# Performance work log

Hardware: AMD Instinct MI355X
Metric: run time of the kernel (lower is better)

The kernel has to match this reference:

```python
import jax, jax.numpy as jnp
import numpy as np

B, CIN, COUT, SDIM, RES, K = 8, 512, 512, 512, 64, 3
AFF_SCALE = 1.0 / np.sqrt(SDIM)          # LinearAct: 1/sqrt(in_features)
CONV_SCALE = 1.0 / np.sqrt(CIN * K * K)  # ModulatedConv2d: 1/sqrt(in*k*k)
LRELU_GAIN = np.sqrt(2.0)                # bias_act 'lrelu' default gain


def setup_inputs() -> dict:
    key = jax.random.key(0)
    k = jax.random.split(key, 5)
    x = jax.random.normal(k[0], (B, CIN, RES, RES), dtype=jnp.float32)
    w = jax.random.normal(k[1], (B, SDIM), dtype=jnp.float32)
    noise = jax.random.normal(k[2], (B, 1, RES, RES), dtype=jnp.float32)
    affine_w = jax.random.normal(k[3], (CIN, SDIM), dtype=jnp.float32)
    affine_b = jnp.ones((CIN,), dtype=jnp.float32)          # bias.data.fill_(1.0)
    conv_w = jax.random.normal(k[4], (COUT, CIN, K, K), dtype=jnp.float32)
    noise_scale = jnp.asarray(0.1, dtype=jnp.float32)        # InjectNoise.scale (nonzero for a meaningful test)
    bias = jnp.zeros((COUT,), dtype=jnp.float32)
    return {"x": x, "w": w, "noise": noise, "affine_w": affine_w,
            "affine_b": affine_b, "conv_w": conv_w,
            "noise_scale": noise_scale, "bias": bias}


def reference(x, w, noise, affine_w, affine_b, conv_w, noise_scale, bias):
    # affine (LinearAct, act='linear'): style = w @ (W*scale)^T + b
    style = jnp.einsum('bs,cs->bc', w, affine_w * AFF_SCALE) + affine_b  # [B, CIN]

    # modulate + demodulate: per-sample weight [B, COUT, CIN, K, K]
    wt = conv_w[None] * style[:, None, :, None, None] * CONV_SCALE
    d = jax.lax.rsqrt(jnp.sum(wt * wt, axis=(2, 3, 4), keepdims=True) + 1e-8)
    wt = wt * d

    # grouped conv (groups=B) == per-sample conv; flip_weight=True -> plain correlation
    def conv_one(xi, wi):
        return jax.lax.conv_general_dilated(
            xi[None], wi, window_strides=(1, 1), padding=[(1, 1), (1, 1)],
            dimension_numbers=('NCHW', 'OIHW', 'NCHW'))[0]

    y = jax.vmap(conv_one)(x, wt)  # [B, COUT, RES, RES]

    # noise -> bias -> lrelu(0.2) * sqrt(2)
    y = y + noise * noise_scale
    y = jax.nn.leaky_relu(y + bias[None, :, None, None], 0.2) * LRELU_GAIN
    return y
```

## Files before the change

kernel.cpp:

```cpp
#include <hip/hip_runtime.h>
#include <hip/hip_bf16.h>

typedef unsigned short u16;

#define BATCH 8
#define CIN 512
#define COUT 512
#define SDIM 512
#define RES 64
#define PIX (RES * RES)
#define PPIX 4356
#define PANEL_E 139392

__device__ __constant__ static const float kAffScale  = 0.04419417382415922f;
__device__ __constant__ static const float kConvScale = 0.014731391274719742f;
__device__ __constant__ static const float kGain      = 1.4142135623730951f;

typedef __bf16 bf16x8 __attribute__((ext_vector_type(8)));
typedef float  f32x4  __attribute__((ext_vector_type(4)));

__global__ void style_k(const float* __restrict__ w, const float* __restrict__ aw,
                        const float* __restrict__ ab, float* __restrict__ style) {
  int tid = blockIdx.x * 256 + threadIdx.x;
  int b = tid >> 9, c = tid & 511;
  const float* wp = w + b * SDIM;
  const float* ap = aw + c * SDIM;
  float s = 0.0f;
  for (int k = 0; k < SDIM; ++k) s += wp[k] * ap[k];
  style[tid] = s * kAffScale + ab[c];
}

__global__ void cw2_k(const float* __restrict__ cw, float* __restrict__ cw2) {
  int tid = blockIdx.x * 256 + threadIdx.x;
  const float* p = cw + tid * 9;
  float s = 0.0f;
  #pragma unroll
  for (int t = 0; t < 9; ++t) { float v = p[t]; s += v * v; }
  cw2[tid] = s;
}

__global__ void fac_k(const float* __restrict__ style, const float* __restrict__ cw2,
                      float* __restrict__ fac) {
  int wid  = blockIdx.x * 4 + (threadIdx.x >> 6);
  int lane = threadIdx.x & 63;
  int b = wid >> 9, o = wid & 511;
  const float* st = style + b * CIN;
  const float* c2 = cw2 + o * CIN;
  float s = 0.0f;
  for (int i = lane; i < CIN; i += 64) { float sv = st[i]; s += sv * sv * c2[i]; }
  #pragma unroll
  for (int off = 32; off; off >>= 1) s += __shfl_xor(s, off);
  if (lane == 0) {
    float d = rsqrtf(s * kConvScale * kConvScale + 1e-8f);
    fac[wid] = d * kConvScale;
  }
}

__global__ void wcast_k(const float* __restrict__ cw, u16* __restrict__ wbt) {
  int tid = blockIdx.x * 256 + threadIdx.x;
  int o = tid >> 9, i = tid & 511;
  const float* p = cw + tid * 9;
  #pragma unroll
  for (int t = 0; t < 9; ++t) {
    __hip_bfloat16 h = __float2bfloat16(p[t]);
    wbt[((size_t)(t * 16 + (i >> 5)) * 512 + o) * 32 + (i & 31)] = *(u16*)&h;
  }
}

__global__ void bz_k(u16* __restrict__ xst) {
  int idx = blockIdx.x * 256 + threadIdx.x;
  if (idx >= 128 * PPIX) return;
  int pan = idx / PPIX, pix = idx - pan * PPIX;
  int h = pix / 66, w = pix - h * 66;
  if (h == 0 || h == 65 || w == 0 || w == 65) {
    u16* p = xst + (size_t)pan * PANEL_E + (size_t)pix * 32;
    int4 z = make_int4(0, 0, 0, 0);
    ((int4*)p)[0] = z; ((int4*)p)[1] = z; ((int4*)p)[2] = z; ((int4*)p)[3] = z;
  }
}

__global__ void modx_k(const float* __restrict__ x, const float* __restrict__ style,
                       u16* __restrict__ xst) {
  __shared__ float t[64][65];
  int b  = blockIdx.z;
  int it = blockIdx.y * 64;
  int pt = blockIdx.x * 64;
  int tp = threadIdx.x & 63;
  int tr = threadIdx.x >> 6;
  for (int r = tr; r < 64; r += 4) {
    int i = it + r;
    t[r][tp] = x[(b * CIN + i) * PIX + pt + tp] * style[b * CIN + i];
  }
  __syncthreads();
  int i = it + tp;
  size_t pbase = (size_t)(b * 16 + (i >> 5)) * PANEL_E + (i & 31);
  for (int r = tr; r < 64; r += 4) {
    int pix = pt + r, h = pix >> 6, w = pix & 63;
    __hip_bfloat16 hh = __float2bfloat16(t[tp][r]);
    xst[pbase + (size_t)((h + 1) * 66 + (w + 1)) * 32] = *(u16*)&hh;
  }
}

__launch_bounds__(512, 2)
__global__ void gemm_k(const u16* __restrict__ wbt, const u16* __restrict__ xst,
                       const float* __restrict__ fac, const float* __restrict__ noise,
                       const float* __restrict__ nscale_p, const float* __restrict__ bias,
                       float* __restrict__ y) {
  __shared__ __align__(16) u16 lds[75264];

  const int tid = threadIdx.x;
  const int bid = blockIdx.x;
  const int swz = (bid & 7) * 32 + (bid >> 3);
  const int mt = swz >> 7;
  const int nt = swz & 127;
  const int b  = nt >> 4;
  const int pimg  = (nt & 15) * 256;
  const int hbase = pimg >> 6;

  const int lane = tid & 63;
  const int wv = tid >> 6;
  const int wm = wv >> 2;
  const int wn = wv & 3;
  const int l15 = lane & 15, l4 = lane >> 4;
  const int pwn = (wn + 1) * 66 + l15;

  int aElem[8];
  #pragma unroll
  for (int mi = 0; mi < 8; ++mi) {
    int arow = wm * 128 + mi * 16 + l15;
    aElem[mi] = arow * 32 + ((l4 ^ ((arow >> 1) & 3)) << 3);
  }

  const int sgE = ((tid & 3) ^ ((tid >> 3) & 3)) << 3;
  int aoffE[2];
  #pragma unroll
  for (int p = 0; p < 2; ++p)
    aoffE[p] = (mt * 256 + ((p * 512 + tid) >> 2)) * 32 + sgE;

  auto stA = [&](int panel, int ring) {
    const u16* pan = wbt + ((size_t)panel << 14);
    #pragma unroll
    for (int p = 0; p < 2; ++p) {
      __builtin_amdgcn_global_load_lds(
          (const __attribute__((address_space(1))) void*)(pan + aoffE[p]),
          (__attribute__((address_space(3))) void*)(&lds[ring * 8192 + (p * 512 + tid) * 8]),
          16, 0, 0);
    }
  };

  auto stHalo = [&](int cbn) {
    const int dst0 = 24576 + (cbn & 1) * 25344;
    const size_t srcPan = (size_t)(b * 16 + cbn * 2) * PANEL_E + (size_t)(hbase * 66) * 32;
    #pragma unroll
    for (int pass = 0; pass < 6; ++pass) {
      int c = pass * 512 + tid;
      int kh = c >= 1584 ? 1 : 0;
      int r = c - (kh ? 1584 : 0);
      int p = r >> 2;
      int sg = (c & 3) ^ ((p >> 1) & 3);
      const u16* src = xst + srcPan + (size_t)kh * PANEL_E + p * 32 + sg * 8;
      __builtin_amdgcn_global_load_lds(
          (const __attribute__((address_space(1))) void*)src,
          (__attribute__((address_space(3))) void*)(&lds[dst0 + c * 8]), 16, 0, 0);
    }
    if (tid < 96) {
      int c = 3072 + tid;
      int p = (c - 1584) >> 2;
      int sg = (c & 3) ^ ((p >> 1) & 3);
      const u16* src = xst + srcPan + (size_t)PANEL_E + p * 32 + sg * 8;
      __builtin_amdgcn_global_load_lds(
          (const __attribute__((address_space(1))) void*)src,
          (__attribute__((address_space(3))) void*)(&lds[dst0 + c * 8]), 16, 0, 0);
    }
  };

  f32x4 acc[8][4];
  #pragma unroll
  for (int i = 0; i < 8; ++i)
    #pragma unroll
    for (int j = 0; j < 4; ++j) acc[i][j] = (f32x4){0.f, 0.f, 0.f, 0.f};

  stHalo(0);
  stA(0, 0);
  stA(1, 1);
  asm volatile("s_waitcnt vmcnt(2)" ::: "memory");
  __builtin_amdgcn_s_barrier();

#define PH(IDX) {                                                              \
    constexpr int tap_ = (IDX) >> 1, kh_ = (IDX) & 1;                          \
    constexpr int rr_ = (IDX) % 3;                                             \
    constexpr int nI_ = (IDX) + 2;                                             \
    constexpr int tapS_ = (nI_ % 18) >> 1, khS_ = (nI_ % 18) & 1;              \
    constexpr int rw_ = nI_ % 3;                                               \
    constexpr int dy_ = tap_ / 3 - 1, dx_ = tap_ % 3 - 1;                      \
    const int sb_ = 24576 + (cb & 1) * 25344 + kh_ * 12672;                    \
    bf16x8 bfr[4], af03[4], af47[4];                                           \
    _Pragma("unroll") for (int ni = 0; ni < 4; ++ni) {                         \
      int prow = pwn + (dy_ * 66 + dx_ + 1 + ni * 16);                         \
      int sl = (l4 ^ ((prow >> 1) & 3)) << 3;                                  \
      bfr[ni] = *(const bf16x8*)&lds[sb_ + prow * 32 + sl];                    \
    }                                                                          \
    _Pragma("unroll") for (int j = 0; j < 4; ++j)                              \
      af03[j] = *(const bf16x8*)&lds[rr_ * 8192 + aElem[j]];                   \
    __builtin_amdgcn_sched_barrier(0);    \
    _Pragma("unroll") for (int j = 0; j < 4; ++j)                              \
      af47[j] = *(const bf16x8*)&lds[rr_ * 8192 + aElem[4 + j]];               \
    stA(tapS_ * 16 + khS_ + ((nI_ >= 18) ? cbw : cb) * 2, rw_);                \
    if ((IDX) == 15) stHalo(cbw);                                              \
    __builtin_amdgcn_s_barrier();                                              \
    asm volatile("s_waitcnt lgkmcnt(4)" ::: "memory");                         \
    __builtin_amdgcn_sched_barrier(0);                                         \
    __builtin_amdgcn_s_setprio(1);                                             \
    _Pragma("unroll") for (int j = 0; j < 4; ++j)                              \
      _Pragma("unroll") for (int ni = 0; ni < 4; ++ni)                         \
        acc[j][ni] = __builtin_amdgcn_mfma_f32_16x16x32_bf16(af03[j], bfr[ni], acc[j][ni], 0, 0, 0); \
    __builtin_amdgcn_s_setprio(0);                                             \
    asm volatile("s_waitcnt lgkmcnt(0)" ::: "memory");                         \
    __builtin_amdgcn_sched_barrier(0);                                         \
    __builtin_amdgcn_s_setprio(1);                                             \
    _Pragma("unroll") for (int j = 0; j < 4; ++j)                              \
      _Pragma("unroll") for (int ni = 0; ni < 4; ++ni)                         \
        acc[4 + j][ni] = __builtin_amdgcn_mfma_f32_16x16x32_bf16(af47[j], bfr[ni], acc[4 + j][ni], 0, 0, 0); \
    __builtin_amdgcn_s_setprio(0);                                             \
    if ((IDX) == 15 || (IDX) == 16) {                                          \
      asm volatile("s_waitcnt vmcnt(8)" ::: "memory");                         \
    } else {                                                                   \
      asm volatile("s_waitcnt vmcnt(2)" ::: "memory");                         \
    }                                                                          \
    __builtin_amdgcn_s_barrier();                                              \
  }

  for (int cb = 0; cb < 8; ++cb) {
    const int cbw = (cb == 7) ? 0 : cb + 1;
    PH(0)  PH(1)  PH(2)  PH(3)  PH(4)  PH(5)  PH(6)  PH(7)  PH(8)
    PH(9)  PH(10) PH(11) PH(12) PH(13) PH(14) PH(15) PH(16) PH(17)
  }
#undef PH

  const float ns = nscale_p[0];
  float nz[4];
  #pragma unroll
  for (int ni = 0; ni < 4; ++ni) {
    int pix = pimg + wn * 64 + ni * 16 + l15;
    nz[ni] = noise[b * PIX + pix] * ns;
  }
  #pragma unroll
  for (int mi = 0; mi < 8; ++mi) {
    int o = mt * 256 + wm * 128 + mi * 16 + l4 * 4;
    f32x4 fv = *(const f32x4*)&fac[b * COUT + o];
    f32x4 bv = *(const f32x4*)&bias[o];
    #pragma unroll
    for (int r = 0; r < 4; ++r) {
      float* yp = y + (size_t)(b * COUT + o + r) * PIX + pimg + wn * 64 + l15;
      #pragma unroll
      for (int ni = 0; ni < 4; ++ni) {
        float v = acc[mi][ni][r] * fv[r] + nz[ni] + bv[r];
        v = (v > 0.0f ? v : 0.2f * v) * kGain;
        yp[ni * 16] = v;
      }
    }
  }
}

extern "C" void kernel_launch(void* const* d_in, const int* in_sizes, int n_in,
                              void* d_out, int out_size, void* d_ws, size_t ws_size,
                              hipStream_t stream) {
  const float* x      = (const float*)d_in[0];
  const float* w      = (const float*)d_in[1];
  const float* noise  = (const float*)d_in[2];
  const float* aff_w  = (const float*)d_in[3];
  const float* aff_b  = (const float*)d_in[4];
  const float* conv_w = (const float*)d_in[5];
  const float* nscale = (const float*)d_in[6];
  const float* bias   = (const float*)d_in[7];
  float* y = (float*)d_out;

  char* ws = (char*)d_ws;
  float* style = (float*)(ws);
  float* fac   = (float*)(ws + 16384);
  float* cw2   = (float*)(ws + 32768);
  u16*   wbt   = (u16*)(ws + 1081600);
  u16*   xst   = (u16*)(ws + 5800192);

  style_k<<<16, 256, 0, stream>>>(w, aff_w, aff_b, style);
  cw2_k<<<1024, 256, 0, stream>>>(conv_w, cw2);
  fac_k<<<1024, 256, 0, stream>>>(style, cw2, fac);
  wcast_k<<<1024, 256, 0, stream>>>(conv_w, wbt);
  bz_k<<<(128 * PPIX + 255) / 256, 256, 0, stream>>>(xst);
  modx_k<<<dim3(64, 8, 8), 256, 0, stream>>>(x, style, xst);
  gemm_k<<<256, 512, 0, stream>>>(wbt, xst, fac, noise, nscale, bias, y);
}
```

Baseline: 191.5 us.

## Load conv activations directly from global into registers instead of staging halo in LDS

Drops the LDS halo staging of the activation panel. Each wave now loads its B fragments straight from global memory into a three-deep register ring (q0/q1/q2), issued two half-phases ahead. The LDS A-weight ring is reorganised to hold both kh halves per tap. This saves LDS capacity and LDS read traffic, but it replaces the shared halo reuse with per-wave global/L2 loads that re-read the overlapping taps, and it keeps more registers live.

```diff
diff --git a/kernel.cpp b/kernel.cpp
--- a/kernel.cpp
+++ b/kernel.cpp
@@ -106,7 +106,7 @@
                        const float* __restrict__ fac, const float* __restrict__ noise,
                        const float* __restrict__ nscale_p, const float* __restrict__ bias,
                        float* __restrict__ y) {
-  __shared__ __align__(16) u16 lds[75264];
+  __shared__ __align__(16) u16 Ab[49152];
 
   const int tid = threadIdx.x;
   const int bid = blockIdx.x;
@@ -122,7 +122,6 @@
   const int wm = wv >> 2;
   const int wn = wv & 3;
   const int l15 = lane & 15, l4 = lane >> 4;
-  const int pwn = (wn + 1) * 66 + l15;
 
   int aElem[8];
   #pragma unroll
@@ -137,105 +136,94 @@
   for (int p = 0; p < 2; ++p)
     aoffE[p] = (mt * 256 + ((p * 512 + tid) >> 2)) * 32 + sgE;
 
-  auto stA = [&](int panel, int ring) {
+  const int pB0 = ((hbase + wn + 1) * 66 + l15 + 1) * 32 + l4 * 8;
+
+  auto stA = [&](int panel, int ring, int khS) {
     const u16* pan = wbt + ((size_t)panel << 14);
     #pragma unroll
     for (int p = 0; p < 2; ++p) {
       __builtin_amdgcn_global_load_lds(
           (const __attribute__((address_space(1))) void*)(pan + aoffE[p]),
-          (__attribute__((address_space(3))) void*)(&lds[ring * 8192 + (p * 512 + tid) * 8]),
+          (__attribute__((address_space(3))) void*)(&Ab[ring * 16384 + khS * 8192 + (p * 512 + tid) * 8]),
           16, 0, 0);
     }
   };
 
-  auto stHalo = [&](int cbn) {
-    const int dst0 = 24576 + (cbn & 1) * 25344;
-    const size_t srcPan = (size_t)(b * 16 + cbn * 2) * PANEL_E + (size_t)(hbase * 66) * 32;
-    #pragma unroll
-    for (int pass = 0; pass < 6; ++pass) {
-      int c = pass * 512 + tid;
-      int kh = c >= 1584 ? 1 : 0;
-      int r = c - (kh ? 1584 : 0);
-      int p = r >> 2;
-      int sg = (c & 3) ^ ((p >> 1) & 3);
-      const u16* src = xst + srcPan + (size_t)kh * PANEL_E + p * 32 + sg * 8;
-      __builtin_amdgcn_global_load_lds(
-          (const __attribute__((address_space(1))) void*)src,
-          (__attribute__((address_space(3))) void*)(&lds[dst0 + c * 8]), 16, 0, 0);
-    }
-    if (tid < 96) {
-      int c = 3072 + tid;
-      int p = (c - 1584) >> 2;
-      int sg = (c & 3) ^ ((p >> 1) & 3);
-      const u16* src = xst + srcPan + (size_t)PANEL_E + p * 32 + sg * 8;
-      __builtin_amdgcn_global_load_lds(
-          (const __attribute__((address_space(1))) void*)src,
-          (__attribute__((address_space(3))) void*)(&lds[dst0 + c * 8]), 16, 0, 0);
-    }
-  };
-
   f32x4 acc[8][4];
   #pragma unroll
   for (int i = 0; i < 8; ++i)
     #pragma unroll
     for (int j = 0; j < 4; ++j) acc[i][j] = (f32x4){0.f, 0.f, 0.f, 0.f};
 
-  stHalo(0);
-  stA(0, 0);
-  stA(1, 1);
-  asm volatile("s_waitcnt vmcnt(2)" ::: "memory");
+  bf16x8 q0[4], q1[4], q2[4];
+
+#define BISSUE(SN, TAPB, CBB, KHB) {                                           \
+    const u16* pb_ = xst + (size_t)(b * 16 + (CBB) * 2 + (KHB)) * PANEL_E      \
+        + ((((TAPB) / 3) - 1) * 66 + ((TAPB) % 3) - 1) * 32 + pB0;             \
+    _Pragma("unroll") for (int ni = 0; ni < 4; ++ni)                           \
+      SN[ni] = *(const bf16x8*)(pb_ + ni * 512);                               \
+  }
+
+#define MFMA16(AF, BQ, MOFF)                                                   \
+    _Pragma("unroll") for (int j = 0; j < 4; ++j)                              \
+      _Pragma("unroll") for (int ni = 0; ni < 4; ++ni)                         \
+        acc[(MOFF) + j][ni] = __builtin_amdgcn_mfma_f32_16x16x32_bf16(         \
+            AF[j], BQ[ni], acc[(MOFF) + j][ni], 0, 0, 0);
+
+  {
+    const int cbw0 = 0;
+    stA(0, 0, 0); stA(1, 0, 1);
+    stA(16, 1, 0); stA(17, 1, 1);
+    BISSUE(q0, 0, cbw0, 0)
+    BISSUE(q1, 0, cbw0, 1)
+  }
+  asm volatile("s_waitcnt vmcnt(4)" ::: "memory");
   __builtin_amdgcn_s_barrier();
 
-#define PH(IDX) {                                                              \
-    constexpr int tap_ = (IDX) >> 1, kh_ = (IDX) & 1;                          \
-    constexpr int rr_ = (IDX) % 3;                                             \
-    constexpr int nI_ = (IDX) + 2;                                             \
-    constexpr int tapS_ = (nI_ % 18) >> 1, khS_ = (nI_ % 18) & 1;              \
-    constexpr int rw_ = nI_ % 3;                                               \
-    constexpr int dy_ = tap_ / 3 - 1, dx_ = tap_ % 3 - 1;                      \
-    const int sb_ = 24576 + (cb & 1) * 25344 + kh_ * 12672;                    \
-    bf16x8 bfr[4], af03[4], af47[4];                                           \
-    _Pragma("unroll") for (int ni = 0; ni < 4; ++ni) {                         \
-      int prow = pwn + (dy_ * 66 + dx_ + 1 + ni * 16);                         \
-      int sl = (l4 ^ ((prow >> 1) & 3)) << 3;                                  \
-      bfr[ni] = *(const bf16x8*)&lds[sb_ + prow * 32 + sl];                    \
-    }                                                                          \
+#define HALF(TAP, KH, SC, SN, TAPB, CBB) {                                     \
+    constexpr int rr_ = (TAP) % 3;                                             \
+    constexpr int rw_ = ((TAP) + 2) % 3;                                       \
+    constexpr int tp2_ = ((TAP) + 2) % 9;                                      \
+    const int cbS_ = ((TAP) < 7) ? cb : cbw;                                   \
+    bf16x8 af03[4], af47[4];                                                   \
     _Pragma("unroll") for (int j = 0; j < 4; ++j)                              \
-      af03[j] = *(const bf16x8*)&lds[rr_ * 8192 + aElem[j]];                   \
-    __builtin_amdgcn_sched_barrier(0);    \
+      af03[j] = *(const bf16x8*)&Ab[rr_ * 16384 + (KH) * 8192 + aElem[j]];     \
+    __builtin_amdgcn_sched_barrier(0);               \
     _Pragma("unroll") for (int j = 0; j < 4; ++j)                              \
-      af47[j] = *(const bf16x8*)&lds[rr_ * 8192 + aElem[4 + j]];               \
-    stA(tapS_ * 16 + khS_ + ((nI_ >= 18) ? cbw : cb) * 2, rw_);                \
-    if ((IDX) == 15) stHalo(cbw);                                              \
+      af47[j] = *(const bf16x8*)&Ab[rr_ * 16384 + (KH) * 8192 + aElem[4 + j]]; \
+    stA(tp2_ * 16 + cbS_ * 2 + (KH), rw_, (KH));                               \
+    BISSUE(SN, TAPB, CBB, KH)                                                  \
+    __builtin_amdgcn_sched_barrier(0);      \
     __builtin_amdgcn_s_barrier();                                              \
     asm volatile("s_waitcnt lgkmcnt(4)" ::: "memory");                         \
     __builtin_amdgcn_sched_barrier(0);                                         \
     __builtin_amdgcn_s_setprio(1);                                             \
-    _Pragma("unroll") for (int j = 0; j < 4; ++j)                              \
-      _Pragma("unroll") for (int ni = 0; ni < 4; ++ni)                         \
-        acc[j][ni] = __builtin_amdgcn_mfma_f32_16x16x32_bf16(af03[j], bfr[ni], acc[j][ni], 0, 0, 0); \
+    MFMA16(af03, SC, 0)                                                        \
     __builtin_amdgcn_s_setprio(0);                                             \
     asm volatile("s_waitcnt lgkmcnt(0)" ::: "memory");                         \
     __builtin_amdgcn_sched_barrier(0);                                         \
     __builtin_amdgcn_s_setprio(1);                                             \
-    _Pragma("unroll") for (int j = 0; j < 4; ++j)                              \
-      _Pragma("unroll") for (int ni = 0; ni < 4; ++ni)                         \
-        acc[4 + j][ni] = __builtin_amdgcn_mfma_f32_16x16x32_bf16(af47[j], bfr[ni], acc[4 + j][ni], 0, 0, 0); \
+    MFMA16(af47, SC, 4)                                                        \
     __builtin_amdgcn_s_setprio(0);                                             \
-    if ((IDX) == 15 || (IDX) == 16) {                                          \
-      asm volatile("s_waitcnt vmcnt(8)" ::: "memory");                         \
-    } else {                                                                   \
-      asm volatile("s_waitcnt vmcnt(2)" ::: "memory");                         \
-    }                                                                          \
+    asm volatile("s_waitcnt vmcnt(6)" ::: "memory");                           \
     __builtin_amdgcn_s_barrier();                                              \
   }
 
   for (int cb = 0; cb < 8; ++cb) {
     const int cbw = (cb == 7) ? 0 : cb + 1;
-    PH(0)  PH(1)  PH(2)  PH(3)  PH(4)  PH(5)  PH(6)  PH(7)  PH(8)
-    PH(9)  PH(10) PH(11) PH(12) PH(13) PH(14) PH(15) PH(16) PH(17)
-  }
-#undef PH
+    HALF(0, 0, q0, q2, 1, cb)  HALF(0, 1, q1, q0, 1, cb)
+    HALF(1, 0, q2, q1, 2, cb)  HALF(1, 1, q0, q2, 2, cb)
+    HALF(2, 0, q1, q0, 3, cb)  HALF(2, 1, q2, q1, 3, cb)
+    HALF(3, 0, q0, q2, 4, cb)  HALF(3, 1, q1, q0, 4, cb)
+    HALF(4, 0, q2, q1, 5, cb)  HALF(4, 1, q0, q2, 5, cb)
+    HALF(5, 0, q1, q0, 6, cb)  HALF(5, 1, q2, q1, 6, cb)
+    HALF(6, 0, q0, q2, 7, cb)  HALF(6, 1, q1, q0, 7, cb)
+    HALF(7, 0, q2, q1, 8, cb)  HALF(7, 1, q0, q2, 8, cb)
+    HALF(8, 0, q1, q0, 0, cbw) HALF(8, 1, q2, q1, 0, cbw)
+  }
+#undef HALF
+#undef MFMA16
+#undef BISSUE
 
   const float ns = nscale_p[0];
   float nz[4];
```

New measurement: 201.0 us. +5.0%, slower.
